# Performance work log

Hardware: AMD Instinct MI355X
Metric: run time of the kernel (lower is better)

Reference implementation:

```python
import jax, jax.numpy as jnp
import numpy as np

B, LQ, LK, D = 16, 2048, 2048, 256
NEG = -1e10


def setup_inputs() -> dict:
    key = jax.random.key(0)
    k1, k2, k3, k4, k5 = jax.random.split(key, 5)
    scale = 1.0 / np.sqrt(D)
    return {
        "x": jax.random.normal(k1, (B, LQ, D), dtype=jnp.float32),
        "y": jax.random.normal(k2, (B, LK, D), dtype=jnp.float32),
        "mask": jnp.zeros((B, LK), dtype=bool),  # True = padded key position
        "Wq": jax.random.normal(k3, (D, D), dtype=jnp.float32) * scale,
        "Wk": jax.random.normal(k4, (D, D), dtype=jnp.float32) * scale,
        "Wv": jax.random.normal(k5, (D, D), dtype=jnp.float32) * scale,
    }


def reference(x, y, mask, Wq, Wk, Wv):
    # nn.Linear: out = in @ W.T (no bias)
    q = jnp.einsum('bqd,ed->bqe', x, Wq)   # [B, LQ, D]
    k = jnp.einsum('bkd,ed->bke', y, Wk)   # [B, LK, D]
    v = jnp.einsum('bkd,ed->bke', y, Wv)   # [B, LK, D]
    # cdist (p=2) via GEMM expansion: ||q||^2 + ||k||^2 - 2 q.k
    qn = jnp.sum(q * q, axis=-1)                              # [B, LQ]
    kn = jnp.sum(k * k, axis=-1)                              # [B, LK]
    d2 = qn[:, :, None] + kn[:, None, :] - 2.0 * jnp.einsum('bqd,bkd->bqk', q, k)
    dist = jnp.sqrt(jnp.maximum(d2, 0.0))                     # [B, LQ, LK]
    scores = jnp.exp(-dist)
    # masked_fill: where original mask is True, set pre-softmax score to -1e10
    scores = jnp.where(mask[:, None, :], NEG, scores)
    attn = jax.nn.softmax(scores, axis=-1)                    # [B, LQ, LK]
    att_out = jnp.einsum('bqk,bkd->bqd', attn, v)             # [B, LQ, D]
    return (att_out, attn)
```

## Files before the change

### kernel.cpp

```cpp
#include <hip/hip_runtime.h>
#include <stdint.h>

#define B_   16
#define L_   2048
#define D_   256
#define NROW (B_*L_)

#define EPAD 40
#define TPAD 66

typedef __attribute__((ext_vector_type(8))) short s8v;
typedef __attribute__((ext_vector_type(4))) float f4v;

__device__ __forceinline__ unsigned short f2b(float f) {
    unsigned u = __builtin_bit_cast(unsigned, f);
    return (unsigned short)((u + 0x7fffu + ((u >> 16) & 1u)) >> 16);
}

__device__ __forceinline__ void gl16(const void* g, void* l) {
    __builtin_amdgcn_global_load_lds(
        (const __attribute__((address_space(1))) unsigned int*)g,
        (__attribute__((address_space(3))) unsigned int*)l, 16, 0, 0);
}

__global__ __launch_bounds__(256) void qkv_kernel(
    const float* __restrict__ x, const float* __restrict__ y,
    const float* __restrict__ Wq, const float* __restrict__ Wk, const float* __restrict__ Wv,
    unsigned short* __restrict__ Qb, unsigned short* __restrict__ Kb,
    unsigned short* __restrict__ Vt,
    float* __restrict__ qn, float* __restrict__ kn)
{
    __shared__ unsigned short Xs[64*256];
    __shared__ unsigned short Ws[64*256];
    __shared__ unsigned short Ts[64*TPAD];

    const int t    = threadIdx.x;
    const int r0   = blockIdx.x * 64;
    const int type = blockIdx.y;

    const float* X = type ? y : x;

    #pragma unroll
    for (int p = 0; p < 16; ++p) {
        int idx  = p*256 + t;
        int row  = idx >> 6;
        int half = idx & 1;
        int blk  = (idx & 63) >> 1;
        int c4   = blk*8 + half*4;
        float4 vx = *(const float4*)(X + (size_t)(r0+row)*D_ + c4);
        uint2 px;
        px.x = (unsigned)f2b(vx.x) | ((unsigned)f2b(vx.y) << 16);
        px.y = (unsigned)f2b(vx.z) | ((unsigned)f2b(vx.w) << 16);
        *(uint2*)(Xs + row*256 + (blk ^ (row & 15))*8 + half*4) = px;
    }

    const int w = t >> 6, lane = t & 63, q16 = lane & 15, quad = lane >> 4;
    const int m0 = w * 16;

    float p4[4] = {0.f, 0.f, 0.f, 0.f};
    const f4v z4 = {0.f, 0.f, 0.f, 0.f};

    for (int ct = 0; ct < 4; ++ct) {
        const int e0 = ct * 64;

        __syncthreads();
        {
            const float* W = type ? Wk : Wq;
            #pragma unroll
            for (int p = 0; p < 16; ++p) {
                int idx  = p*256 + t;
                int row  = idx >> 6;
                int half = idx & 1;
                int blk  = (idx & 63) >> 1;
                int c4   = blk*8 + half*4;
                float4 vw = *(const float4*)(W + (size_t)(e0+row)*D_ + c4);
                uint2 pw;
                pw.x = (unsigned)f2b(vw.x) | ((unsigned)f2b(vw.y) << 16);
                pw.y = (unsigned)f2b(vw.z) | ((unsigned)f2b(vw.w) << 16);
                *(uint2*)(Ws + row*256 + (blk ^ (row & 15))*8 + half*4) = pw;
            }
        }
        __syncthreads();

        f4v acc[4];
        #pragma unroll
        for (int n = 0; n < 4; ++n) acc[n] = z4;
        #pragma unroll
        for (int c = 0; c < 8; ++c) {
            s8v a = *(const s8v*)(Xs + (m0 + q16)*256 + (((c*4+quad) ^ q16)*8));
            #pragma unroll
            for (int n = 0; n < 4; ++n) {
                s8v bb = *(const s8v*)(Ws + (n*16 + q16)*256 + (((c*4+quad) ^ q16)*8));
                acc[n] = __builtin_amdgcn_mfma_f32_16x16x32_bf16(a, bb, acc[n], 0, 0, 0);
            }
        }
        {
            unsigned short* Out = type ? Kb : Qb;
            #pragma unroll
            for (int n = 0; n < 4; ++n)
                #pragma unroll
                for (int r = 0; r < 4; ++r) {
                    float v = acc[n][r];
                    p4[r] += v * v;
                    Out[(size_t)(r0 + m0 + quad*4 + r)*D_ + e0 + n*16 + q16] = f2b(v);
                }
        }

        if (type) {
            __syncthreads();
            #pragma unroll
            for (int p = 0; p < 16; ++p) {
                int idx  = p*256 + t;
                int row  = idx >> 6;
                int half = idx & 1;
                int blk  = (idx & 63) >> 1;
                int c4   = blk*8 + half*4;
                float4 vw = *(const float4*)(Wv + (size_t)(e0+row)*D_ + c4);
                uint2 pw;
                pw.x = (unsigned)f2b(vw.x) | ((unsigned)f2b(vw.y) << 16);
                pw.y = (unsigned)f2b(vw.z) | ((unsigned)f2b(vw.w) << 16);
                *(uint2*)(Ws + row*256 + (blk ^ (row & 15))*8 + half*4) = pw;
            }
            __syncthreads();

            f4v vacc[4];
            #pragma unroll
            for (int n = 0; n < 4; ++n) vacc[n] = z4;
            #pragma unroll
            for (int c = 0; c < 8; ++c) {
                s8v a = *(const s8v*)(Xs + (m0 + q16)*256 + (((c*4+quad) ^ q16)*8));
                #pragma unroll
                for (int n = 0; n < 4; ++n) {
                    s8v bb = *(const s8v*)(Ws + (n*16 + q16)*256 + (((c*4+quad) ^ q16)*8));
                    vacc[n] = __builtin_amdgcn_mfma_f32_16x16x32_bf16(a, bb, vacc[n], 0, 0, 0);
                }
            }
            #pragma unroll
            for (int n = 0; n < 4; ++n)
                #pragma unroll
                for (int r = 0; r < 4; ++r)
                    Ts[(m0 + quad*4 + r)*TPAD + n*16 + q16] = f2b(vacc[n][r]);
            __syncthreads();
            int j    = t >> 2;
            int kseg = t & 3;
            unsigned pk[8];
            #pragma unroll
            for (int i = 0; i < 8; ++i) {
                unsigned lo = Ts[(kseg*16 + 2*i    )*TPAD + j];
                unsigned hi = Ts[(kseg*16 + 2*i + 1)*TPAD + j];
                pk[i] = lo | (hi << 16);
            }
            int bb_ = r0 >> 11;
            int k0g = r0 & (L_ - 1);
            unsigned short* dst = Vt + (size_t)(bb_*D_ + e0 + j)*L_ + k0g + kseg*16;
            *(uint4*)dst       = make_uint4(pk[0], pk[1], pk[2], pk[3]);
            *((uint4*)dst + 1) = make_uint4(pk[4], pk[5], pk[6], pk[7]);
        }
    }

    {
        float* norm = type ? kn : qn;
        #pragma unroll
        for (int r = 0; r < 4; ++r) {
            float v = p4[r];
            v += __shfl_xor(v, 1, 16);
            v += __shfl_xor(v, 2, 16);
            v += __shfl_xor(v, 4, 16);
            v += __shfl_xor(v, 8, 16);
            if (q16 == 0) norm[r0 + m0 + quad*4 + r] = v;
        }
    }
}

__device__ __forceinline__ void stage_K(const unsigned short* Kb, unsigned short* ks,
                                        int bk, int k0, int w, int lane) {
    #pragma unroll
    for (int p = 0; p < 4; ++p) {
        int slot = p*256 + w*64 + lane;
        int row  = slot >> 5;
        int blk  = slot & 31;
        gl16(Kb + (size_t)(bk + k0 + row)*D_ + ((blk ^ (row & 15))*8),
             ks + (size_t)(p*256 + w*64)*8);
    }
}
__device__ __forceinline__ void stage_V(const unsigned short* Vt, unsigned short* vs,
                                        int bD, int k0, int w, int lane) {
    #pragma unroll
    for (int p = 0; p < 4; ++p) {
        int slot = p*256 + w*64 + lane;
        int d    = slot >> 2;
        int blk  = slot & 3;
        gl16(Vt + (size_t)(bD + d)*L_ + k0 + ((blk ^ ((d >> 1) & 3))*8),
             vs + (size_t)(p*256 + w*64)*8);
    }
}

__global__ __launch_bounds__(256) void attnpv_kernel(
    const unsigned short* __restrict__ Qb, const unsigned short* __restrict__ Kb,
    const unsigned short* __restrict__ Vt,
    const float* __restrict__ qn, const float* __restrict__ kn,
    const unsigned char* __restrict__ mask,
    float* __restrict__ rowsum, float* __restrict__ att_out)
{
    __shared__ unsigned short Ks[2][32*256];
    __shared__ unsigned short Vs[2][256*32];
    __shared__ unsigned short Es[4][16*EPAD];

    const int t  = threadIdx.x;
    const int q0 = blockIdx.x * 64;
    const int b  = blockIdx.y;
    const int bk = b * L_;
    const int bD = b * D_;
    const int w = t >> 6, lane = t & 63, q16 = lane & 15, quad = lane >> 4;

    const int qrow = bk + q0 + w*16;
    s8v qa[8];
    float qnr[4];
    #pragma unroll
    for (int c = 0; c < 8; ++c)
        qa[c] = *(const s8v*)(Qb + (size_t)(qrow + q16)*D_ + c*32 + quad*8);
    #pragma unroll
    for (int r = 0; r < 4; ++r)
        qnr[r] = qn[qrow + quad*4 + r];

    float rs[4] = {0.f, 0.f, 0.f, 0.f};
    const f4v z4 = {0.f, 0.f, 0.f, 0.f};
    f4v O[16];
    #pragma unroll
    for (int n = 0; n < 16; ++n) O[n] = z4;

    stage_K(Kb, Ks[0], bk, 0, w, lane);
    stage_V(Vt, Vs[0], bD, 0, w, lane);
    for (int kt = 0; kt < 64; ++kt) {
        const int k0 = kt * 32;
        const int cur = kt & 1;
        __syncthreads();
        if (kt < 63) {
            stage_K(Kb, Ks[cur ^ 1], bk, k0 + 32, w, lane);
            stage_V(Vt, Vs[cur ^ 1], bD, k0 + 32, w, lane);
        }

        float kcv[2]; int mkv[2];
        #pragma unroll
        for (int n = 0; n < 2; ++n) {
            kcv[n] = kn[bk + k0 + n*16 + q16];
            mkv[n] = mask[bk + k0 + n*16 + q16];
        }

        #pragma unroll
        for (int n = 0; n < 2; ++n) {
            f4v s = {0.f, 0.f, 0.f, 0.f};
            #pragma unroll
            for (int c = 0; c < 8; ++c) {
                s8v bb = *(const s8v*)(Ks[cur] + (n*16 + q16)*256 + (((c*4+quad) ^ q16)*8));
                s = __builtin_amdgcn_mfma_f32_16x16x32_bf16(qa[c], bb, s, 0, 0, 0);
            }
            #pragma unroll
            for (int r = 0; r < 4; ++r) {
                float d2 = qnr[r] + kcv[n] - 2.0f * s[r];
                float dist = sqrtf(fmaxf(d2, 0.f));
                float E = mkv[n] ? 0.f : __expf(__expf(-dist));
                rs[r] += E;
                Es[w][(quad*4 + r)*EPAD + n*16 + q16] =
                    (unsigned short)(__builtin_bit_cast(unsigned, E) >> 16);
            }
        }
        s8v af = *(const s8v*)(&Es[w][q16*EPAD + quad*8]);
        #pragma unroll
        for (int n = 0; n < 16; ++n) {
            s8v vb = *(const s8v*)(Vs[cur] + (n*16 + q16)*32 +
                                   ((quad ^ ((q16 >> 1) & 3))*8));
            O[n] = __builtin_amdgcn_mfma_f32_16x16x32_bf16(af, vb, O[n], 0, 0, 0);
        }
    }

    float inv[4];
    #pragma unroll
    for (int r = 0; r < 4; ++r) {
        float v = rs[r];
        v += __shfl_xor(v, 1, 16);
        v += __shfl_xor(v, 2, 16);
        v += __shfl_xor(v, 4, 16);
        v += __shfl_xor(v, 8, 16);
        if (q16 == 0) rowsum[qrow + quad*4 + r] = v;
        inv[r] = 1.0f / v;
    }

    #pragma unroll
    for (int n = 0; n < 16; ++n)
        #pragma unroll
        for (int r = 0; r < 4; ++r)
            att_out[(size_t)(qrow + quad*4 + r)*D_ + n*16 + q16] = O[n][r] * inv[r];
}

__global__ __launch_bounds__(256) void attnw_kernel(
    const unsigned short* __restrict__ Qb, const unsigned short* __restrict__ Kb,
    const float* __restrict__ qn, const float* __restrict__ kn,
    const float* __restrict__ rowsum,
    const unsigned char* __restrict__ mask,
    float* __restrict__ attn_out)
{
    __shared__ unsigned short Ks[2][32*256];

    const int t  = threadIdx.x;
    const int q0 = blockIdx.x * 64;
    const int b  = blockIdx.y;
    const int bk = b * L_;
    const int kbase = blockIdx.z * 1024;
    const int w = t >> 6, lane = t & 63, q16 = lane & 15, quad = lane >> 4;

    const int qrow = bk + q0 + w*16;
    s8v qa[8];
    float qnr[4], inv[4];
    #pragma unroll
    for (int c = 0; c < 8; ++c)
        qa[c] = *(const s8v*)(Qb + (size_t)(qrow + q16)*D_ + c*32 + quad*8);
    #pragma unroll
    for (int r = 0; r < 4; ++r) {
        qnr[r] = qn[qrow + quad*4 + r];
        inv[r] = 1.0f / rowsum[qrow + quad*4 + r];
    }

    stage_K(Kb, Ks[0], bk, kbase, w, lane);
    for (int kt = 0; kt < 32; ++kt) {
        const int k0 = kbase + kt*32;
        const int cur = kt & 1;
        __syncthreads();
        if (kt < 31) stage_K(Kb, Ks[cur ^ 1], bk, k0 + 32, w, lane);

        float kcv[2]; int mkv[2];
        #pragma unroll
        for (int n = 0; n < 2; ++n) {
            kcv[n] = kn[bk + k0 + n*16 + q16];
            mkv[n] = mask[bk + k0 + n*16 + q16];
        }
        #pragma unroll
        for (int n = 0; n < 2; ++n) {
            f4v s = {0.f, 0.f, 0.f, 0.f};
            #pragma unroll
            for (int c = 0; c < 8; ++c) {
                s8v bb = *(const s8v*)(Ks[cur] + (n*16 + q16)*256 + (((c*4+quad) ^ q16)*8));
                s = __builtin_amdgcn_mfma_f32_16x16x32_bf16(qa[c], bb, s, 0, 0, 0);
            }
            #pragma unroll
            for (int r = 0; r < 4; ++r) {
                float d2 = qnr[r] + kcv[n] - 2.0f * s[r];
                float dist = sqrtf(fmaxf(d2, 0.f));
                float E = mkv[n] ? 0.f : __expf(__expf(-dist));
                attn_out[(size_t)(qrow + quad*4 + r)*L_ + k0 + n*16 + q16] = E * inv[r];
            }
        }
    }
}

extern "C" void kernel_launch(void* const* d_in, const int* in_sizes, int n_in,
                              void* d_out, int out_size, void* d_ws, size_t ws_size,
                              hipStream_t stream) {
    (void)in_sizes; (void)n_in; (void)out_size; (void)ws_size;
    const float* x  = (const float*)d_in[0];
    const float* y  = (const float*)d_in[1];
    const unsigned char* mask = (const unsigned char*)d_in[2];
    const float* Wq = (const float*)d_in[3];
    const float* Wk = (const float*)d_in[4];
    const float* Wv = (const float*)d_in[5];

    char* ws = (char*)d_ws;
    unsigned short* Qb = (unsigned short*)ws;
    unsigned short* Kb = Qb + (size_t)NROW * D_;
    unsigned short* Vt = Kb + (size_t)NROW * D_;
    float* qn     = (float*)(ws + 3 * (size_t)NROW * D_ * 2);
    float* kn     = qn + NROW;
    float* rowsum = kn + NROW;

    float* att_out = (float*)d_out;
    float* attn    = att_out + (size_t)NROW * D_;

    qkv_kernel<<<dim3(512, 2), 256, 0, stream>>>(x, y, Wq, Wk, Wv,
                                                 Qb, Kb, Vt, qn, kn);
    attnpv_kernel<<<dim3(32, 16), 256, 0, stream>>>(Qb, Kb, Vt, qn, kn, mask,
                                                    rowsum, att_out);
    attnw_kernel<<<dim3(32, 16, 2), 256, 0, stream>>>(Qb, Kb, qn, kn, rowsum,
                                                      mask, attn);
}
```

Measured before the change: 636.1 us.

## Store unnormalized bf16 scores from PV pass and normalize them in a light kernel

The attention-weight kernel no longer recomputes QK^T, the distance and the double exponential. The PV kernel now writes its bf16 unnormalized score tile to a workspace buffer, and a simple elementwise kernel scales it by the inverse row sum into the fp32 attn output. This removes the second QK GEMM and the transcendental work. In exchange it adds a 128MB bf16 write and read, and the attn output carries bf16 precision. The score rounding also changes from truncation to round-to-nearest.

```diff
diff --git a/kernel.cpp b/kernel.cpp
--- a/kernel.cpp
+++ b/kernel.cpp
@@ -200,6 +200,7 @@
     const unsigned short* __restrict__ Vt,
     const float* __restrict__ qn, const float* __restrict__ kn,
     const unsigned char* __restrict__ mask,
+    unsigned short* __restrict__ Eb,
     float* __restrict__ rowsum, float* __restrict__ att_out)
 {
     __shared__ unsigned short Ks[2][32*256];
@@ -222,6 +223,9 @@
     #pragma unroll
     for (int r = 0; r < 4; ++r)
         qnr[r] = qn[qrow + quad*4 + r];
+
+    unsigned short* ebase = Eb + (size_t)(qrow + (lane >> 2))*L_ + (lane & 3)*8;
+    const unsigned short* esrc = &Es[w][(lane >> 2)*EPAD + (lane & 3)*8];
 
     float rs[4] = {0.f, 0.f, 0.f, 0.f};
     const f4v z4 = {0.f, 0.f, 0.f, 0.f};
@@ -261,8 +265,7 @@
                 float dist = sqrtf(fmaxf(d2, 0.f));
                 float E = mkv[n] ? 0.f : __expf(__expf(-dist));
                 rs[r] += E;
-                Es[w][(quad*4 + r)*EPAD + n*16 + q16] =
-                    (unsigned short)(__builtin_bit_cast(unsigned, E) >> 16);
+                Es[w][(quad*4 + r)*EPAD + n*16 + q16] = f2b(E);
             }
         }
         s8v af = *(const s8v*)(&Es[w][q16*EPAD + quad*8]);
@@ -272,6 +275,7 @@
                                    ((quad ^ ((q16 >> 1) & 3))*8));
             O[n] = __builtin_amdgcn_mfma_f32_16x16x32_bf16(af, vb, O[n], 0, 0, 0);
         }
+        *(s8v*)(ebase + k0) = *(const s8v*)esrc;
     }
 
     float inv[4];
@@ -293,64 +297,28 @@
             att_out[(size_t)(qrow + quad*4 + r)*D_ + n*16 + q16] = O[n][r] * inv[r];
 }
 
-__global__ __launch_bounds__(256) void attnw_kernel(
-    const unsigned short* __restrict__ Qb, const unsigned short* __restrict__ Kb,
-    const float* __restrict__ qn, const float* __restrict__ kn,
+__global__ __launch_bounds__(256) void norm_kernel(
+    const unsigned short* __restrict__ Eb,
     const float* __restrict__ rowsum,
-    const unsigned char* __restrict__ mask,
     float* __restrict__ attn_out)
 {
-    __shared__ unsigned short Ks[2][32*256];
-
-    const int t  = threadIdx.x;
-    const int q0 = blockIdx.x * 64;
-    const int b  = blockIdx.y;
-    const int bk = b * L_;
-    const int kbase = blockIdx.z * 1024;
-    const int w = t >> 6, lane = t & 63, q16 = lane & 15, quad = lane >> 4;
-
-    const int qrow = bk + q0 + w*16;
-    s8v qa[8];
-    float qnr[4], inv[4];
-    #pragma unroll
-    for (int c = 0; c < 8; ++c)
-        qa[c] = *(const s8v*)(Qb + (size_t)(qrow + q16)*D_ + c*32 + quad*8);
-    #pragma unroll
-    for (int r = 0; r < 4; ++r) {
-        qnr[r] = qn[qrow + quad*4 + r];
-        inv[r] = 1.0f / rowsum[qrow + quad*4 + r];
-    }
-
-    stage_K(Kb, Ks[0], bk, kbase, w, lane);
-    for (int kt = 0; kt < 32; ++kt) {
-        const int k0 = kbase + kt*32;
-        const int cur = kt & 1;
-        __syncthreads();
-        if (kt < 31) stage_K(Kb, Ks[cur ^ 1], bk, k0 + 32, w, lane);
-
-        float kcv[2]; int mkv[2];
-        #pragma unroll
-        for (int n = 0; n < 2; ++n) {
-            kcv[n] = kn[bk + k0 + n*16 + q16];
-            mkv[n] = mask[bk + k0 + n*16 + q16];
-        }
-        #pragma unroll
-        for (int n = 0; n < 2; ++n) {
-            f4v s = {0.f, 0.f, 0.f, 0.f};
-            #pragma unroll
-            for (int c = 0; c < 8; ++c) {
-                s8v bb = *(const s8v*)(Ks[cur] + (n*16 + q16)*256 + (((c*4+quad) ^ q16)*8));
-                s = __builtin_amdgcn_mfma_f32_16x16x32_bf16(qa[c], bb, s, 0, 0, 0);
-            }
-            #pragma unroll
-            for (int r = 0; r < 4; ++r) {
-                float d2 = qnr[r] + kcv[n] - 2.0f * s[r];
-                float dist = sqrtf(fmaxf(d2, 0.f));
-                float E = mkv[n] ? 0.f : __expf(__expf(-dist));
-                attn_out[(size_t)(qrow + quad*4 + r)*L_ + k0 + n*16 + q16] = E * inv[r];
-            }
-        }
-    }
+    const int row = blockIdx.x;
+    const int t   = threadIdx.x;
+    const float inv = 1.0f / rowsum[row];
+    const size_t base = (size_t)row * L_ + t*8;
+
+    s8v e = *(const s8v*)(Eb + base);
+    float4 o0, o1;
+    o0.x = __builtin_bit_cast(float, ((unsigned)(unsigned short)e[0]) << 16) * inv;
+    o0.y = __builtin_bit_cast(float, ((unsigned)(unsigned short)e[1]) << 16) * inv;
+    o0.z = __builtin_bit_cast(float, ((unsigned)(unsigned short)e[2]) << 16) * inv;
+    o0.w = __builtin_bit_cast(float, ((unsigned)(unsigned short)e[3]) << 16) * inv;
+    o1.x = __builtin_bit_cast(float, ((unsigned)(unsigned short)e[4]) << 16) * inv;
+    o1.y = __builtin_bit_cast(float, ((unsigned)(unsigned short)e[5]) << 16) * inv;
+    o1.z = __builtin_bit_cast(float, ((unsigned)(unsigned short)e[6]) << 16) * inv;
+    o1.w = __builtin_bit_cast(float, ((unsigned)(unsigned short)e[7]) << 16) * inv;
+    *(float4*)(attn_out + base)     = o0;
+    *(float4*)(attn_out + base + 4) = o1;
 }
 
 extern "C" void kernel_launch(void* const* d_in, const int* in_sizes, int n_in,
@@ -371,6 +339,7 @@
     float* qn     = (float*)(ws + 3 * (size_t)NROW * D_ * 2);
     float* kn     = qn + NROW;
     float* rowsum = kn + NROW;
+    unsigned short* Eb = (unsigned short*)(rowsum + NROW);
 
     float* att_out = (float*)d_out;
     float* attn    = att_out + (size_t)NROW * D_;
@@ -378,7 +347,6 @@
     qkv_kernel<<<dim3(512, 2), 256, 0, stream>>>(x, y, Wq, Wk, Wv,
                                                  Qb, Kb, Vt, qn, kn);
     attnpv_kernel<<<dim3(32, 16), 256, 0, stream>>>(Qb, Kb, Vt, qn, kn, mask,
-                                                    rowsum, att_out);
-    attnw_kernel<<<dim3(32, 16, 2), 256, 0, stream>>>(Qb, Kb, qn, kn, rowsum,
-                                                      mask, attn);
-}
+                                                    Eb, rowsum, att_out);
+    norm_kernel<<<dim3(NROW), 256, 0, stream>>>(Eb, rowsum, attn);
+}
```

Result: faster. 590.7 us (-7.1%).
